# Optimization experiments

Measured on AMD Instinct MI355X. Metric: run time of the kernel, lower is better.

## Reference

```python
import jax, jax.numpy as jnp
import numpy as np

D_MODEL = 768
N_HEADS = 12
D_K = D_MODEL // N_HEADS
NEG_INF = -1e9


def setup_inputs() -> dict:
    key = jax.random.key(0)
    ks = jax.random.split(key, 7)
    B, S = 4, 2048
    x = jax.random.normal(ks[0], (B, S, D_MODEL), dtype=jnp.float32)
    # causal mask, broadcastable to [B, H, S, S]
    mask = jnp.tril(jnp.ones((S, S), dtype=bool))[None, None, :, :]
    scale = 1.0 / np.sqrt(D_MODEL)
    Wq = jax.random.normal(ks[1], (D_MODEL, D_MODEL), dtype=jnp.float32) * scale
    bq = jnp.zeros((D_MODEL,), dtype=jnp.float32)
    Wk = jax.random.normal(ks[2], (D_MODEL, D_MODEL), dtype=jnp.float32) * scale
    bk = jnp.zeros((D_MODEL,), dtype=jnp.float32)
    Wv = jax.random.normal(ks[3], (D_MODEL, D_MODEL), dtype=jnp.float32) * scale
    bv = jnp.zeros((D_MODEL,), dtype=jnp.float32)
    return {"x": x, "mask": mask, "Wq": Wq, "bq": bq, "Wk": Wk, "bk": bk, "Wv": Wv, "bv": bv}


def reference(x, mask, Wq, bq, Wk, bk, Wv, bv):
    B, S, _ = x.shape
    # projections (torch Linear: y = x @ W.T + b)
    q = (x @ Wq.T + bq).reshape(B, S, N_HEADS, D_K)
    k = (x @ Wk.T + bk).reshape(B, S, N_HEADS, D_K)
    v = (x @ Wv.T + bv).reshape(B, S, N_HEADS, D_K)
    # scores: [B, H, S, S]
    scores = jnp.einsum("bqhd,bkhd->bhqk", q, k) / jnp.sqrt(jnp.float32(D_K))
    scores = jnp.where(mask, scores, NEG_INF)
    probs = jax.nn.softmax(scores, axis=-1)
    # attention: [B, H, S, D_K] -> [B, S, d_model]
    attn = jnp.einsum("bhqk,bkhd->bqhd", probs, v).reshape(B, S, D_MODEL)
    return attn
```

## Files before the change

kernel.cpp:

```cpp
#include <hip/hip_runtime.h>


#define S_LEN 2048
#define BATCH 4
#define HEADS 12
#define DM 768
#define DK 64
#define BH (BATCH*HEADS)
#define MROWS (BATCH*S_LEN)

typedef __attribute__((ext_vector_type(8))) short short8;
typedef __attribute__((ext_vector_type(4))) float floatx4;
typedef __attribute__((address_space(3))) unsigned char lds_byte;
typedef __attribute__((address_space(1))) const unsigned char glob_byte;

__device__ __forceinline__ unsigned short f2bf(float f) {
  union { float f; unsigned int u; } a; a.f = f;
  unsigned int u = a.u;
  return (unsigned short)((u + 0x7fffu + ((u >> 16) & 1u)) >> 16);
}

__global__ void cast_f32_bf16(const float* __restrict__ src,
                              unsigned short* __restrict__ dst, int n) {
  int i = (blockIdx.x * blockDim.x + threadIdx.x) * 4;
  if (i < n) {
    float4 v = *(const float4*)(src + i);
    ushort4 o;
    o.x = f2bf(v.x); o.y = f2bf(v.y); o.z = f2bf(v.z); o.w = f2bf(v.w);
    *(ushort4*)(dst + i) = o;
  }
}

__global__ void cast_w3(const float* __restrict__ w0, const float* __restrict__ w1,
                        const float* __restrict__ w2, unsigned short* __restrict__ dst,
                        int n) {
  const float* src = (blockIdx.y == 0) ? w0 : (blockIdx.y == 1) ? w1 : w2;
  int i = (blockIdx.x * blockDim.x + threadIdx.x) * 4;
  if (i < n) {
    float4 v = *(const float4*)(src + i);
    ushort4 o;
    o.x = f2bf(v.x); o.y = f2bf(v.y); o.z = f2bf(v.z); o.w = f2bf(v.w);
    *(ushort4*)(dst + (size_t)blockIdx.y * n + i) = o;
  }
}

__global__ __launch_bounds__(256) void qkv_gemm(
    const unsigned short* __restrict__ xb,
    const unsigned short* __restrict__ wb,
    const float* __restrict__ bq, const float* __restrict__ bk,
    const float* __restrict__ bv,
    unsigned short* __restrict__ qo,
    unsigned short* __restrict__ ko,
    unsigned short* __restrict__ vto) {
  __shared__ unsigned short a_lds[128 * 32];
  __shared__ unsigned short b_lds[128 * 32];
  const int mat = blockIdx.z;
  const int tid = threadIdx.x;
  const int wave = tid >> 6, lane = tid & 63, quad = lane >> 4, ln = lane & 15;
  const int wm = wave & 1, wn = wave >> 1;
  const int m_blk = blockIdx.x * 128, n_blk = blockIdx.y * 128;
  const unsigned short* w = wb + (size_t)mat * DM * DM;

  const int srow = lane >> 2, schunk = lane & 3;

  const floatx4 fz = {0.f, 0.f, 0.f, 0.f};
  floatx4 acc[4][4];
#pragma unroll
  for (int mg = 0; mg < 4; mg++)
#pragma unroll
    for (int c = 0; c < 4; c++) acc[mg][c] = fz;

  for (int k0 = 0; k0 < DM; k0 += 32) {
#pragma unroll
    for (int j = 0; j < 2; j++) {
      int row = wave * 32 + j * 16 + srow;
      __builtin_amdgcn_global_load_lds(
          (glob_byte*)(xb + (size_t)(m_blk + row) * DM + k0 + schunk * 8),
          (lds_byte*)(a_lds + (size_t)(wave * 32 + j * 16) * 32), 16, 0, 0);
      __builtin_amdgcn_global_load_lds(
          (glob_byte*)(w + (size_t)(n_blk + row) * DM + k0 + schunk * 8),
          (lds_byte*)(b_lds + (size_t)(wave * 32 + j * 16) * 32), 16, 0, 0);
    }
    __syncthreads();

    short8 af[4], bf[4];
#pragma unroll
    for (int mg = 0; mg < 4; mg++)
      af[mg] = *(const short8*)(a_lds + (wm * 64 + mg * 16 + ln) * 32 + quad * 8);
#pragma unroll
    for (int c = 0; c < 4; c++)
      bf[c] = *(const short8*)(b_lds + (wn * 64 + c * 16 + ln) * 32 + quad * 8);
#pragma unroll
    for (int mg = 0; mg < 4; mg++)
#pragma unroll
      for (int c = 0; c < 4; c++)
        acc[mg][c] = __builtin_amdgcn_mfma_f32_16x16x32_bf16(af[mg], bf[c], acc[mg][c], 0, 0, 0);
    __syncthreads();
  }

  const float* bias = (mat == 0) ? bq : (mat == 1) ? bk : bv;
  const int m_base = m_blk + wm * 64, n_base = n_blk + wn * 64;
#pragma unroll
  for (int mg = 0; mg < 4; mg++)
#pragma unroll
    for (int c = 0; c < 4; c++) {
      int gn = n_base + c * 16 + ln;
      int hd = gn >> 6, d = gn & 63;
      float bias_v = bias[gn];
      int gm0 = m_base + mg * 16 + quad * 4;
      int bb = gm0 >> 11, s0 = gm0 & (S_LEN - 1);
      if (mat == 2) {
        ushort4 pk;
        pk.x = f2bf(acc[mg][c][0] + bias_v);
        pk.y = f2bf(acc[mg][c][1] + bias_v);
        pk.z = f2bf(acc[mg][c][2] + bias_v);
        pk.w = f2bf(acc[mg][c][3] + bias_v);
        *(ushort4*)(vto + (((size_t)(bb * HEADS + hd)) * DK + d) * S_LEN + s0) = pk;
      } else {
        unsigned short* dst = (mat == 0 ? qo : ko) +
            (((size_t)(bb * HEADS + hd)) * S_LEN + s0) * DK + d;
#pragma unroll
        for (int r = 0; r < 4; r++)
          dst[(size_t)r * DK] = f2bf(acc[mg][c][r] + bias_v);
      }
    }
}

__global__ __launch_bounds__(128) void flash_attn(
    const unsigned short* __restrict__ q,
    const unsigned short* __restrict__ k,
    const unsigned short* __restrict__ vt,
    float* __restrict__ out) {
  __shared__ unsigned short p_lds[2][32 * 64];
  const int id = blockIdx.x;
  const int bh = id % BH;
  const int qt = (S_LEN / 64 - 1) - (id / BH);
  const int q0 = qt * 64;
  const int tid = threadIdx.x;
  const int wave = tid >> 6, lane = tid & 63, quad = lane >> 4, ln = lane & 15;
  unsigned short* pl = p_lds[wave];
  const unsigned short* qp = q  + (size_t)bh * S_LEN * DK;
  const unsigned short* kp = k  + (size_t)bh * S_LEN * DK;
  const unsigned short* vp = vt + (size_t)bh * DK * S_LEN;
  const int qr_base = q0 + wave * 32;

  short8 aq[2][2];
#pragma unroll
  for (int h = 0; h < 2; h++)
#pragma unroll
    for (int s = 0; s < 2; s++)
      aq[h][s] = *(const short8*)(qp + (size_t)(qr_base + h * 16 + ln) * DK + s * 32 + quad * 8);

  const floatx4 fz = {0.f, 0.f, 0.f, 0.f};
  floatx4 o[2][4];
  float l_part[2][4];
#pragma unroll
  for (int h = 0; h < 2; h++)
#pragma unroll
    for (int r = 0; r < 4; r++) {
      o[h][0] = fz; o[h][1] = fz; o[h][2] = fz; o[h][3] = fz;
      l_part[h][r] = 0.f;
    }

  const int kend = qr_base + 32;
  for (int k0 = 0; k0 < kend; k0 += 64) {
    short8 kf[4][2];
#pragma unroll
    for (int kg = 0; kg < 4; kg++)
#pragma unroll
      for (int s = 0; s < 2; s++)
        kf[kg][s] = *(const short8*)(kp + (size_t)(k0 + kg * 16 + ln) * DK + s * 32 + quad * 8);

    floatx4 sc[2][4];
#pragma unroll
    for (int h = 0; h < 2; h++)
#pragma unroll
      for (int kg = 0; kg < 4; kg++) {
        floatx4 t = __builtin_amdgcn_mfma_f32_16x16x32_bf16(aq[h][0], kf[kg][0], fz, 0, 0, 0);
        sc[h][kg] = __builtin_amdgcn_mfma_f32_16x16x32_bf16(aq[h][1], kf[kg][1], t, 0, 0, 0);
      }

    const bool domask = (k0 + 63 > qr_base);
#pragma unroll
    for (int h = 0; h < 2; h++) {
#pragma unroll
      for (int kg = 0; kg < 4; kg++) {
        int key = k0 + kg * 16 + ln;
#pragma unroll
        for (int r = 0; r < 4; r++) {
          float p = __expf(sc[h][kg][r] * 0.125f);
          if (domask) {
            int qr = qr_base + h * 16 + quad * 4 + r;
            p = (key <= qr) ? p : 0.f;
          }
          l_part[h][r] += p;
          int row = h * 16 + quad * 4 + r;
          int col = kg * 16 + ln;
          pl[row * 64 + (((col >> 3) ^ (row & 7)) * 8) + (col & 7)] = f2bf(p);
        }
      }
    }

    short8 ap[2][2];
#pragma unroll
    for (int h = 0; h < 2; h++)
#pragma unroll
      for (int s = 0; s < 2; s++)
        ap[h][s] = *(const short8*)(pl + (h * 16 + ln) * 64 + (((s * 4 + quad) ^ (ln & 7)) * 8));

    short8 vf[4][2];
#pragma unroll
    for (int dg = 0; dg < 4; dg++)
#pragma unroll
      for (int s = 0; s < 2; s++)
        vf[dg][s] = *(const short8*)(vp + (size_t)(dg * 16 + ln) * S_LEN + k0 + s * 32 + quad * 8);
#pragma unroll
    for (int h = 0; h < 2; h++)
#pragma unroll
      for (int dg = 0; dg < 4; dg++) {
        o[h][dg] = __builtin_amdgcn_mfma_f32_16x16x32_bf16(ap[h][0], vf[dg][0], o[h][dg], 0, 0, 0);
        o[h][dg] = __builtin_amdgcn_mfma_f32_16x16x32_bf16(ap[h][1], vf[dg][1], o[h][dg], 0, 0, 0);
      }
  }

  const int b = bh / HEADS, hd = bh % HEADS;
#pragma unroll
  for (int h = 0; h < 2; h++)
#pragma unroll
    for (int r = 0; r < 4; r++) {
      float l = l_part[h][r];
      l += __shfl_xor(l, 1);
      l += __shfl_xor(l, 2);
      l += __shfl_xor(l, 4);
      l += __shfl_xor(l, 8);
      float inv = 1.f / l;
      int qr = qr_base + h * 16 + quad * 4 + r;
      float* orow = out + ((size_t)(b * S_LEN + qr)) * DM + hd * DK;
      orow[ln]      = o[h][0][r] * inv;
      orow[16 + ln] = o[h][1][r] * inv;
      orow[32 + ln] = o[h][2][r] * inv;
      orow[48 + ln] = o[h][3][r] * inv;
    }
}

extern "C" void kernel_launch(void* const* d_in, const int* in_sizes, int n_in,
                              void* d_out, int out_size, void* d_ws, size_t ws_size,
                              hipStream_t stream) {
  const float* x  = (const float*)d_in[0];
  const float* Wq = (const float*)d_in[2];
  const float* bq = (const float*)d_in[3];
  const float* Wk = (const float*)d_in[4];
  const float* bk = (const float*)d_in[5];
  const float* Wv = (const float*)d_in[6];
  const float* bv = (const float*)d_in[7];
  float* out = (float*)d_out;

  const int NX = MROWS * DM;
  const int NW = DM * DM;
  unsigned short* xb = (unsigned short*)d_ws;
  unsigned short* wb = xb + NX;
  unsigned short* qo = wb + 3 * NW;
  unsigned short* ko = qo + (size_t)BH * S_LEN * DK;
  unsigned short* vt = ko + (size_t)BH * S_LEN * DK;

  cast_f32_bf16<<<(NX / 4 + 255) / 256, 256, 0, stream>>>(x, xb, NX);
  cast_w3<<<dim3((NW / 4 + 255) / 256, 3), 256, 0, stream>>>(Wq, Wk, Wv, wb, NW);

  qkv_gemm<<<dim3(MROWS / 128, DM / 128, 3), 256, 0, stream>>>(
      xb, wb, bq, bk, bv, qo, ko, vt);

  flash_attn<<<dim3((S_LEN / 64) * BH), 128, 0, stream>>>(qo, ko, vt, out);
}
```

Measured before the change: 254.8 us.

## Fold softmax scale into Q, use exp2, compute row sums via MFMA

```diff
diff --git a/kernel.cpp b/kernel.cpp
--- a/kernel.cpp
+++ b/kernel.cpp
@@ -1,4 +1,5 @@
 #include <hip/hip_runtime.h>
+#include <math.h>
 
 
 #define S_LEN 2048
@@ -8,6 +9,7 @@
 #define DK 64
 #define BH (BATCH*HEADS)
 #define MROWS (BATCH*S_LEN)
+#define QSCALE 0.1803368801111244f
 
 typedef __attribute__((ext_vector_type(8))) short short8;
 typedef __attribute__((ext_vector_type(4))) float floatx4;
@@ -18,6 +20,10 @@
   union { float f; unsigned int u; } a; a.f = f;
   unsigned int u = a.u;
   return (unsigned short)((u + 0x7fffu + ((u >> 16) & 1u)) >> 16);
+}
+__device__ __forceinline__ unsigned short f2bf_rtz(float f) {
+  union { float f; unsigned int u; } a; a.f = f;
+  return (unsigned short)(a.u >> 16);
 }
 
 __global__ void cast_f32_bf16(const float* __restrict__ src,
@@ -60,7 +66,6 @@
   const int wm = wave & 1, wn = wave >> 1;
   const int m_blk = blockIdx.x * 128, n_blk = blockIdx.y * 128;
   const unsigned short* w = wb + (size_t)mat * DM * DM;
-
   const int srow = lane >> 2, schunk = lane & 3;
 
   const floatx4 fz = {0.f, 0.f, 0.f, 0.f};
@@ -99,6 +104,7 @@
   }
 
   const float* bias = (mat == 0) ? bq : (mat == 1) ? bk : bv;
+  const float oscale = (mat == 0) ? QSCALE : 1.0f;
   const int m_base = m_blk + wm * 64, n_base = n_blk + wn * 64;
 #pragma unroll
   for (int mg = 0; mg < 4; mg++)
@@ -106,7 +112,7 @@
     for (int c = 0; c < 4; c++) {
       int gn = n_base + c * 16 + ln;
       int hd = gn >> 6, d = gn & 63;
-      float bias_v = bias[gn];
+      float bias_v = bias[gn] * oscale;
       int gm0 = m_base + mg * 16 + quad * 4;
       int bb = gm0 >> 11, s0 = gm0 & (S_LEN - 1);
       if (mat == 2) {
@@ -121,7 +127,7 @@
             (((size_t)(bb * HEADS + hd)) * S_LEN + s0) * DK + d;
 #pragma unroll
         for (int r = 0; r < 4; r++)
-          dst[(size_t)r * DK] = f2bf(acc[mg][c][r] + bias_v);
+          dst[(size_t)r * DK] = f2bf(acc[mg][c][r] * oscale + bias_v);
       }
     }
 }
@@ -143,24 +149,37 @@
   const unsigned short* kp = k  + (size_t)bh * S_LEN * DK;
   const unsigned short* vp = vt + (size_t)bh * DK * S_LEN;
   const int qr_base = q0 + wave * 32;
+  const floatx4 fz = {0.f, 0.f, 0.f, 0.f};
+
+  unsigned short* wp[4];
+#pragma unroll
+  for (int kg = 0; kg < 4; kg++)
+    wp[kg] = pl + quad * 256 + (((((kg ^ quad) & 3) << 1) | (ln >> 3)) * 8) + (ln & 7);
+  const unsigned short* rp[2];
+#pragma unroll
+  for (int ss = 0; ss < 2; ss++)
+    rp[ss] = pl + ln * 64 + (((ss * 4 + quad) ^ (((ln >> 2) & 3) << 1)) * 8);
+
+  const int klane = ln * DK + quad * 8;
+  const int vlane = ln * S_LEN + quad * 8;
+
+  short8 ones;
+#pragma unroll
+  for (int j = 0; j < 8; j++) ones[j] = (short)0x3F80;
 
   short8 aq[2][2];
 #pragma unroll
   for (int h = 0; h < 2; h++)
 #pragma unroll
-    for (int s = 0; s < 2; s++)
-      aq[h][s] = *(const short8*)(qp + (size_t)(qr_base + h * 16 + ln) * DK + s * 32 + quad * 8);
-
-  const floatx4 fz = {0.f, 0.f, 0.f, 0.f};
+    for (int ss = 0; ss < 2; ss++)
+      aq[h][ss] = *(const short8*)(qp + (qr_base + h * 16 + ln) * DK + ss * 32 + quad * 8);
+
   floatx4 o[2][4];
-  float l_part[2][4];
-#pragma unroll
-  for (int h = 0; h < 2; h++)
-#pragma unroll
-    for (int r = 0; r < 4; r++) {
-      o[h][0] = fz; o[h][1] = fz; o[h][2] = fz; o[h][3] = fz;
-      l_part[h][r] = 0.f;
-    }
+  floatx4 ol[2] = {fz, fz};
+#pragma unroll
+  for (int h = 0; h < 2; h++) {
+    o[h][0] = fz; o[h][1] = fz; o[h][2] = fz; o[h][3] = fz;
+  }
 
   const int kend = qr_base + 32;
   for (int k0 = 0; k0 < kend; k0 += 64) {
@@ -168,59 +187,59 @@
 #pragma unroll
     for (int kg = 0; kg < 4; kg++)
 #pragma unroll
-      for (int s = 0; s < 2; s++)
-        kf[kg][s] = *(const short8*)(kp + (size_t)(k0 + kg * 16 + ln) * DK + s * 32 + quad * 8);
+      for (int ss = 0; ss < 2; ss++)
+        kf[kg][ss] = *(const short8*)(kp + klane + (k0 + kg * 16) * DK + ss * 32);
 
     floatx4 sc[2][4];
 #pragma unroll
     for (int h = 0; h < 2; h++)
 #pragma unroll
       for (int kg = 0; kg < 4; kg++) {
-        floatx4 t = __builtin_amdgcn_mfma_f32_16x16x32_bf16(aq[h][0], kf[kg][0], fz, 0, 0, 0);
-        sc[h][kg] = __builtin_amdgcn_mfma_f32_16x16x32_bf16(aq[h][1], kf[kg][1], t, 0, 0, 0);
-      }
+        floatx4 tt = __builtin_amdgcn_mfma_f32_16x16x32_bf16(aq[h][0], kf[kg][0], fz, 0, 0, 0);
+        sc[h][kg] = __builtin_amdgcn_mfma_f32_16x16x32_bf16(aq[h][1], kf[kg][1], tt, 0, 0, 0);
+      }
+
+    short8 vf[4][2];
+#pragma unroll
+    for (int dg = 0; dg < 4; dg++)
+#pragma unroll
+      for (int ss = 0; ss < 2; ss++)
+        vf[dg][ss] = *(const short8*)(vp + vlane + dg * 16 * S_LEN + k0 + ss * 32);
 
     const bool domask = (k0 + 63 > qr_base);
 #pragma unroll
-    for (int h = 0; h < 2; h++) {
+    for (int h = 0; h < 2; h++)
 #pragma unroll
       for (int kg = 0; kg < 4; kg++) {
         int key = k0 + kg * 16 + ln;
 #pragma unroll
         for (int r = 0; r < 4; r++) {
-          float p = __expf(sc[h][kg][r] * 0.125f);
+          float pv = exp2f(sc[h][kg][r]);
           if (domask) {
             int qr = qr_base + h * 16 + quad * 4 + r;
-            p = (key <= qr) ? p : 0.f;
+            pv = (key <= qr) ? pv : 0.f;
           }
-          l_part[h][r] += p;
-          int row = h * 16 + quad * 4 + r;
-          int col = kg * 16 + ln;
-          pl[row * 64 + (((col >> 3) ^ (row & 7)) * 8) + (col & 7)] = f2bf(p);
+          wp[kg][h * 1024 + r * 64] = f2bf_rtz(pv);
         }
       }
-    }
 
     short8 ap[2][2];
 #pragma unroll
     for (int h = 0; h < 2; h++)
 #pragma unroll
-      for (int s = 0; s < 2; s++)
-        ap[h][s] = *(const short8*)(pl + (h * 16 + ln) * 64 + (((s * 4 + quad) ^ (ln & 7)) * 8));
-
-    short8 vf[4][2];
-#pragma unroll
-    for (int dg = 0; dg < 4; dg++)
-#pragma unroll
-      for (int s = 0; s < 2; s++)
-        vf[dg][s] = *(const short8*)(vp + (size_t)(dg * 16 + ln) * S_LEN + k0 + s * 32 + quad * 8);
-#pragma unroll
-    for (int h = 0; h < 2; h++)
+      for (int ss = 0; ss < 2; ss++)
+        ap[h][ss] = *(const short8*)(rp[ss] + h * 1024);
+
+#pragma unroll
+    for (int h = 0; h < 2; h++) {
 #pragma unroll
       for (int dg = 0; dg < 4; dg++) {
         o[h][dg] = __builtin_amdgcn_mfma_f32_16x16x32_bf16(ap[h][0], vf[dg][0], o[h][dg], 0, 0, 0);
         o[h][dg] = __builtin_amdgcn_mfma_f32_16x16x32_bf16(ap[h][1], vf[dg][1], o[h][dg], 0, 0, 0);
       }
+      ol[h] = __builtin_amdgcn_mfma_f32_16x16x32_bf16(ap[h][0], ones, ol[h], 0, 0, 0);
+      ol[h] = __builtin_amdgcn_mfma_f32_16x16x32_bf16(ap[h][1], ones, ol[h], 0, 0, 0);
+    }
   }
 
   const int b = bh / HEADS, hd = bh % HEADS;
@@ -228,12 +247,7 @@
   for (int h = 0; h < 2; h++)
 #pragma unroll
     for (int r = 0; r < 4; r++) {
-      float l = l_part[h][r];
-      l += __shfl_xor(l, 1);
-      l += __shfl_xor(l, 2);
-      l += __shfl_xor(l, 4);
-      l += __shfl_xor(l, 8);
-      float inv = 1.f / l;
+      float inv = 1.f / ol[h][r];
       int qr = qr_base + h * 16 + quad * 4 + r;
       float* orow = out + ((size_t)(b * S_LEN + qr)) * DM + hd * DK;
       orow[ln]      = o[h][0][r] * inv;
```

After: 254.8 us. No clear change (-0.0%).
